# Optimization experiments

Hardware: AMD Instinct MI355X
Metric: run time of the kernel (lower is better)

Reference implementation:

```python
import jax, jax.numpy as jnp
import numpy as np

TOTAL_POINTS = 1048576
C = 256
B = 512


def setup_inputs() -> dict:
    key = jax.random.key(0)
    k1, k2 = jax.random.split(key)
    values = jax.random.normal(k1, (TOTAL_POINTS, C), dtype=jnp.float32)
    # sorted segment ids == flattened ragged list membership (List[(N_i,C)])
    segment_ids = jnp.sort(jax.random.randint(k2, (TOTAL_POINTS,), 0, B, dtype=jnp.int32))
    return {"values": values, "segment_ids": segment_ids, "num_segments": B}


def reference(values, segment_ids, num_segments):
    # torch.stack([x.sum(dim=0) for x in inputs]) == segmented sum over the
    # flattened point axis -> (B, C). Single fused pass, indices are sorted.
    return jax.ops.segment_sum(values, segment_ids,
                               num_segments=num_segments,
                               indices_are_sorted=True)
```

## Files before the change

### kernel.cpp

```cpp
#include <hip/hip_runtime.h>


#define TOTAL_POINTS 1048576
#define NCOLS 256
#define NSEGS 512
#define NBLOCKS 2048
#define ROWS_PER_BLOCK (TOTAL_POINTS / NBLOCKS)

typedef float v4 __attribute__((ext_vector_type(4)));

__global__ __launch_bounds__(256) void segsum_kernel(
    const v4* __restrict__ vals,
    const int* __restrict__ segids,
    float* __restrict__ out)
{
    const int c4 = threadIdx.x & 63;
    const int rg = threadIdx.x >> 6;
    const long r0 = (long)blockIdx.x * ROWS_PER_BLOCK;

    const int segFirst = segids[r0];
    const int segLast  = segids[r0 + ROWS_PER_BLOCK - 1];

    v4 acc = (v4)(0.f);

    if (segFirst == segLast) {
        const v4* p = vals + (r0 + rg) * 64 + c4;
        #pragma unroll 8
        for (int i = 0; i < ROWS_PER_BLOCK / 4; ++i) {
            acc += __builtin_nontemporal_load(p);
            p += 4 * 64;
        }
        float* o = out + (long)segFirst * NCOLS + c4 * 4;
        atomicAdd(o + 0, acc.x);
        atomicAdd(o + 1, acc.y);
        atomicAdd(o + 2, acc.z);
        atomicAdd(o + 3, acc.w);
        return;
    }

    int cur = -1;
    for (int i = rg; i < ROWS_PER_BLOCK; i += 4) {
        const long row = r0 + i;
        const int seg = segids[row];
        if (seg != cur) {
            if (cur >= 0) {
                float* o = out + (long)cur * NCOLS + c4 * 4;
                atomicAdd(o + 0, acc.x);
                atomicAdd(o + 1, acc.y);
                atomicAdd(o + 2, acc.z);
                atomicAdd(o + 3, acc.w);
            }
            cur = seg;
            acc = (v4)(0.f);
        }
        acc += __builtin_nontemporal_load(&vals[row * 64 + c4]);
    }
    if (cur >= 0) {
        float* o = out + (long)cur * NCOLS + c4 * 4;
        atomicAdd(o + 0, acc.x);
        atomicAdd(o + 1, acc.y);
        atomicAdd(o + 2, acc.z);
        atomicAdd(o + 3, acc.w);
    }
}

extern "C" void kernel_launch(void* const* d_in, const int* in_sizes, int n_in,
                              void* d_out, int out_size, void* d_ws, size_t ws_size,
                              hipStream_t stream) {
    const float* vals = (const float*)d_in[0];
    const int* segids = (const int*)d_in[1];
    float* out = (float*)d_out;

    hipMemsetAsync(out, 0, (size_t)out_size * sizeof(float), stream);

    segsum_kernel<<<NBLOCKS, 256, 0, stream>>>(
        (const v4*)vals, segids, out);
}
```

Measured before the change: 1.358 ms.

## Partition work by segment via binary search instead of fixed row chunks

Each block is now assigned a quarter of one segment, with the segment bounds found by a dual binary search over the sorted ids. This removes the per-row segment id reads and the branchy boundary handling, so every block runs a uniform streaming sum. Nontemporal loads become plain loads. The cost is about 20 dependent global reads per block for the search, plus load imbalance when segment sizes differ.

Measured after the change: 1.330 ms. 2.1% less time.

```diff
diff --git a/kernel.cpp b/kernel.cpp
--- a/kernel.cpp
+++ b/kernel.cpp
@@ -4,8 +4,8 @@
 #define TOTAL_POINTS 1048576
 #define NCOLS 256
 #define NSEGS 512
-#define NBLOCKS 2048
-#define ROWS_PER_BLOCK (TOTAL_POINTS / NBLOCKS)
+#define SPLIT 4
+#define NBLOCKS (NSEGS * SPLIT)
 
 typedef float v4 __attribute__((ext_vector_type(4)));
 
@@ -16,47 +16,37 @@
 {
     const int c4 = threadIdx.x & 63;
     const int rg = threadIdx.x >> 6;
-    const long r0 = (long)blockIdx.x * ROWS_PER_BLOCK;
+    const int seg = blockIdx.x >> 2;
+    const int q   = blockIdx.x & 3;
 
-    const int segFirst = segids[r0];
-    const int segLast  = segids[r0 + ROWS_PER_BLOCK - 1];
+    int lo0 = 0, hi0 = TOTAL_POINTS;
+    int lo1 = 0, hi1 = TOTAL_POINTS;
+    #pragma unroll
+    for (int it = 0; it < 20; ++it) {
+        const int m0 = (lo0 + hi0) >> 1;
+        const int m1 = (lo1 + hi1) >> 1;
+        const int a = segids[m0];
+        const int b = segids[m1];
+        if (a < seg)     lo0 = m0 + 1; else hi0 = m0;
+        if (b < seg + 1) lo1 = m1 + 1; else hi1 = m1;
+    }
+    const int rows   = lo1 - lo0;
+    const int rstart = lo0 + ((rows * q) >> 2);
+    const int rend   = lo0 + ((rows * (q + 1)) >> 2);
+
+    const int n = rend - (rstart + rg);
+    const int iters = (n > 0) ? ((n + 3) >> 2) : 0;
 
     v4 acc = (v4)(0.f);
-
-    if (segFirst == segLast) {
-        const v4* p = vals + (r0 + rg) * 64 + c4;
-        #pragma unroll 8
-        for (int i = 0; i < ROWS_PER_BLOCK / 4; ++i) {
-            acc += __builtin_nontemporal_load(p);
-            p += 4 * 64;
-        }
-        float* o = out + (long)segFirst * NCOLS + c4 * 4;
-        atomicAdd(o + 0, acc.x);
-        atomicAdd(o + 1, acc.y);
-        atomicAdd(o + 2, acc.z);
-        atomicAdd(o + 3, acc.w);
-        return;
+    const v4* p = vals + (long)(rstart + rg) * 64 + c4;
+    #pragma unroll 8
+    for (int i = 0; i < iters; ++i) {
+        acc += p[0];
+        p += 4 * 64;
     }
 
-    int cur = -1;
-    for (int i = rg; i < ROWS_PER_BLOCK; i += 4) {
-        const long row = r0 + i;
-        const int seg = segids[row];
-        if (seg != cur) {
-            if (cur >= 0) {
-                float* o = out + (long)cur * NCOLS + c4 * 4;
-                atomicAdd(o + 0, acc.x);
-                atomicAdd(o + 1, acc.y);
-                atomicAdd(o + 2, acc.z);
-                atomicAdd(o + 3, acc.w);
-            }
-            cur = seg;
-            acc = (v4)(0.f);
-        }
-        acc += __builtin_nontemporal_load(&vals[row * 64 + c4]);
-    }
-    if (cur >= 0) {
-        float* o = out + (long)cur * NCOLS + c4 * 4;
+    if (iters > 0) {
+        float* o = out + (long)seg * NCOLS + (c4 << 2);
         atomicAdd(o + 0, acc.x);
         atomicAdd(o + 1, acc.y);
         atomicAdd(o + 2, acc.z);
```
